# Kernel tuning notes

Hardware: AMD Instinct MI355X
Metric: run time of the kernel (lower is better)

Reference implementation:

```python
import jax, jax.numpy as jnp
import numpy as np

TOPK = (1, 5)


def setup_inputs() -> dict:
    key = jax.random.key(0)
    kZ, kY, kI = jax.random.split(key, 3)
    b, s, f = 9600, 2400, 4096
    Z = jax.random.normal(kZ, (b, f), dtype=jnp.float32)
    Y = jax.random.normal(kY, (s, f), dtype=jnp.float32)
    y_idxs = jax.random.randint(kI, (b,), 0, s, dtype=jnp.int64 if jax.config.jax_enable_x64 else jnp.int32)
    test_y_idxs = jnp.arange(s, dtype=y_idxs.dtype)
    return {"Z": Z, "y_idxs": y_idxs, "Y": Y, "test_y_idxs": test_y_idxs}


def reference(Z, y_idxs, Y, test_y_idxs):
    # L2-normalize rows, then cosine similarity as a single GEMM instead of the
    # original broadcasted (b, s, f) F.cosine_similarity intermediate.
    eps = 1e-8
    Zn = Z / jnp.maximum(jnp.linalg.norm(Z, axis=-1, keepdims=True), eps)
    Yn = Y / jnp.maximum(jnp.linalg.norm(Y, axis=-1, keepdims=True), eps)
    similarity = Zn @ Yn.T  # (b, s)

    # labels[i] = position of y_idxs[i] inside test_y_idxs (each appears exactly once)
    labels = jnp.argmax(y_idxs[None, :] == test_y_idxs[:, None], axis=0)  # (b,)

    accs = []
    for k in TOPK:
        _, topk_idx = jax.lax.top_k(similarity, k)  # (b, k)
        hit = jnp.any(topk_idx == labels[:, None], axis=1)
        accs.append(jnp.mean(hit.astype(jnp.float32)))
    return jnp.stack(accs)
```

## Files before the change

### kernel.cpp

```cpp
#include <hip/hip_runtime.h>

#define INT_MAX_C 0x7fffffff

typedef __attribute__((ext_vector_type(8))) short s16x8;
typedef __attribute__((ext_vector_type(4))) float f32x4;

__global__ void k_init_inv(int* inv, int s) {
  int j = blockIdx.x * 256 + threadIdx.x;
  if (j < s) inv[j] = INT_MAX_C;
}

__global__ void k_scatter(const int* __restrict__ tyi, int* __restrict__ inv, int s) {
  int j = blockIdx.x * 256 + threadIdx.x;
  if (j < s) {
    int v = tyi[j];
    if (v >= 0 && v < s) atomicMin(&inv[v], j);
  }
}

__global__ void k_labels(const int* __restrict__ yi, const int* __restrict__ inv,
                         int* __restrict__ labels, int b, int s) {
  int i = blockIdx.x * 256 + threadIdx.x;
  if (i < b) {
    int v = yi[i];
    int lab = 0;
    if (v >= 0 && v < s) { int p = inv[v]; if (p != INT_MAX_C) lab = p; }
    labels[i] = lab;
  }
}

__global__ __launch_bounds__(256) void k_ynorm(const float* __restrict__ Y,
                                               float* __restrict__ invY, int f) {
  int j = blockIdx.x;
  const float* row = Y + (size_t)j * f;
  float ss = 0.f;
  for (int k = threadIdx.x * 4; k < f; k += 256 * 4) {
    float4 v = *(const float4*)(row + k);
    ss += v.x * v.x + v.y * v.y + v.z * v.z + v.w * v.w;
  }
  int lane = threadIdx.x & 63, wid = threadIdx.x >> 6;
#pragma unroll
  for (int o = 32; o > 0; o >>= 1) ss += __shfl_down(ss, o, 64);
  __shared__ float sh[4];
  if (lane == 0) sh[wid] = ss;
  __syncthreads();
  if (threadIdx.x == 0) {
    float tot = sh[0] + sh[1] + sh[2] + sh[3];
    invY[j] = 1.f / fmaxf(sqrtf(tot), 1e-8f);
  }
}

__global__ __launch_bounds__(256) void k_zrow(
    const float* __restrict__ Z, const float* __restrict__ Y,
    const int* __restrict__ labels, const float* __restrict__ invY,
    float* __restrict__ invZ, float* __restrict__ simL, int f) {
  int i = blockIdx.x;
  int lab = labels[i];
  const float* zr = Z + (size_t)i * f;
  const float* yr = Y + (size_t)lab * f;
  float ss = 0.f, dt = 0.f;
  for (int k = threadIdx.x * 4; k < f; k += 256 * 4) {
    float4 z = *(const float4*)(zr + k);
    float4 y = *(const float4*)(yr + k);
    ss += z.x * z.x + z.y * z.y + z.z * z.z + z.w * z.w;
    dt += z.x * y.x + z.y * y.y + z.z * y.z + z.w * y.w;
  }
  int lane = threadIdx.x & 63, wid = threadIdx.x >> 6;
#pragma unroll
  for (int o = 32; o > 0; o >>= 1) {
    ss += __shfl_down(ss, o, 64);
    dt += __shfl_down(dt, o, 64);
  }
  __shared__ float shs[4], shd[4];
  if (lane == 0) { shs[wid] = ss; shd[wid] = dt; }
  __syncthreads();
  if (threadIdx.x == 0) {
    float S = shs[0] + shs[1] + shs[2] + shs[3];
    float D = shd[0] + shd[1] + shd[2] + shd[3];
    float iz = 1.f / fmaxf(sqrtf(S), 1e-8f);
    invZ[i] = iz;
    simL[i] = D * iz * invY[lab];
  }
}

__device__ __forceinline__ uint rne_hi_bits(uint u) {
  return (u + 0x7fffu + ((u >> 16) & 1u)) & 0xffff0000u;
}

__device__ __forceinline__ void split_pack8(float4 a, float4 b, uint4& hi, uint4& lo) {
  float v[8] = {a.x, a.y, a.z, a.w, b.x, b.y, b.z, b.w};
  uint h[8], l[8];
#pragma unroll
  for (int i = 0; i < 8; ++i) {
    uint u = __float_as_uint(v[i]);
    uint rh = rne_hi_bits(u);
    h[i] = rh;
    float d = v[i] - __uint_as_float(rh);
    uint ud = __float_as_uint(d);
    l[i] = (ud + 0x7fffu + ((ud >> 16) & 1u));
  }
  hi = make_uint4((h[0] >> 16) | h[1], (h[2] >> 16) | h[3],
                  (h[4] >> 16) | h[5], (h[6] >> 16) | h[7]);
  lo = make_uint4((l[0] >> 16) | (l[1] & 0xffff0000u),
                  (l[2] >> 16) | (l[3] & 0xffff0000u),
                  (l[4] >> 16) | (l[5] & 0xffff0000u),
                  (l[6] >> 16) | (l[7] & 0xffff0000u));
}

__global__ __launch_bounds__(256) void k_packZ(const float* __restrict__ Z,
                                               const float* __restrict__ Y,
                                               const int* __restrict__ labels,
                                               const float* __restrict__ invY,
                                               char* __restrict__ Zpan,
                                               float* __restrict__ invZ,
                                               float* __restrict__ simL,
                                               int f, int nkc) {
  int r = blockIdx.x * 4 + (threadIdx.x >> 6);
  int lane = threadIdx.x & 63;
  int rt = r >> 7, rl = r & 127;
  char* pan = Zpan + (size_t)rt * nkc * 16384;
  const float* row = Z + (size_t)r * f;
  int lab = labels[r];
  const float* yrow = Y + (size_t)lab * f;
  float ss = 0.f, dt = 0.f;
  int niter = f >> 9;
  for (int j = 0; j < niter; ++j) {
    int gq = lane + 64 * j;
    float4 v0 = *(const float4*)(row + gq * 8);
    float4 v1 = *(const float4*)(row + gq * 8 + 4);
    float4 y0 = *(const float4*)(yrow + gq * 8);
    float4 y1 = *(const float4*)(yrow + gq * 8 + 4);
    ss += v0.x * v0.x + v0.y * v0.y + v0.z * v0.z + v0.w * v0.w +
          v1.x * v1.x + v1.y * v1.y + v1.z * v1.z + v1.w * v1.w;
    dt += v0.x * y0.x + v0.y * y0.y + v0.z * y0.z + v0.w * y0.w +
          v1.x * y1.x + v1.y * y1.y + v1.z * y1.z + v1.w * y1.w;
    uint4 h, l;
    split_pack8(v0, v1, h, l);
    int kc = gq >> 2, kq = gq & 3;
    size_t off = (size_t)kc * 16384 + rl * 64 + ((kq ^ ((rl >> 1) & 3)) << 4);
    *(uint4*)(pan + off) = h;
    *(uint4*)(pan + off + 8192) = l;
  }
#pragma unroll
  for (int o = 32; o > 0; o >>= 1) {
    ss += __shfl_down(ss, o, 64);
    dt += __shfl_down(dt, o, 64);
  }
  if (lane == 0) {
    float iz = 1.f / fmaxf(sqrtf(ss), 1e-8f);
    invZ[r] = iz;
    simL[r] = dt * iz * invY[lab];
  }
}

__global__ __launch_bounds__(256) void k_packY(const float* __restrict__ Y,
                                               char* __restrict__ Ypan,
                                               float* __restrict__ invY,
                                               int s, int f, int nkc) {
  int r = blockIdx.x * 4 + (threadIdx.x >> 6);
  int lane = threadIdx.x & 63;
  int ct = r / 160, rl = r % 160;
  char* pan = Ypan + (size_t)ct * nkc * 20480;
  const float* row = Y + (size_t)r * f;
  const bool ok = r < s;
  float ss = 0.f;
  int niter = f >> 9;
  for (int j = 0; j < niter; ++j) {
    int gq = lane + 64 * j;
    float4 v0 = {}, v1 = {};
    if (ok) {
      v0 = *(const float4*)(row + gq * 8);
      v1 = *(const float4*)(row + gq * 8 + 4);
    }
    ss += v0.x * v0.x + v0.y * v0.y + v0.z * v0.z + v0.w * v0.w +
          v1.x * v1.x + v1.y * v1.y + v1.z * v1.z + v1.w * v1.w;
    uint4 h, l;
    split_pack8(v0, v1, h, l);
    int kc = gq >> 2, kq = gq & 3;
    size_t off = (size_t)kc * 20480 + rl * 64 + ((kq ^ ((rl >> 1) & 3)) << 4);
    *(uint4*)(pan + off) = h;
    *(uint4*)(pan + off + 10240) = l;
  }
  if (ok) {
#pragma unroll
    for (int o = 32; o > 0; o >>= 1) ss += __shfl_down(ss, o, 64);
    if (lane == 0) invY[r] = 1.f / fmaxf(sqrtf(ss), 1e-8f);
  }
}

__device__ __forceinline__ void dma16(const void* g, void* l) {
  __builtin_amdgcn_global_load_lds((const __attribute__((address_space(1))) unsigned int*)g,
                                   (__attribute__((address_space(3))) unsigned int*)l,
                                   16, 0, 0);
}

__global__ __launch_bounds__(256, 3) void k_gemm_rank_pan(
    const char* __restrict__ Zpan, const char* __restrict__ Ypan,
    const float* __restrict__ invZ, const float* __restrict__ invY,
    const float* __restrict__ simL, const int* __restrict__ labels,
    int* __restrict__ rank, int b, int s, int nkc) {
  __shared__ ushort SMu[18432];
  char* SMb = (char*)SMu;
  __shared__ float sL[128], sIz[128];
  __shared__ int sLab[128], sCnt[128];

  const int t = threadIdx.x;
  const int row0 = blockIdx.x * 128;
  const int col0 = blockIdx.y * 160;

  if (t < 128) {
    int gi = row0 + t;
    sL[t] = simL[gi]; sIz[t] = invZ[gi]; sLab[t] = labels[gi];
    sCnt[t] = 0;
  }

  const char* srcA = Zpan + (size_t)blockIdx.x * nkc * 16384 + t * 16;
  const char* srcB = Ypan + (size_t)blockIdx.y * nkc * 20480 + t * 16;

  const int lane = t & 63;
  const int wv = t >> 6;
  const int wr = wv >> 1, wc = wv & 1;
  const int fm = lane & 15, quad = lane >> 4;

  int aoff[4], boff[5];
#pragma unroll
  for (int i = 0; i < 4; ++i) {
    int r = wr * 64 + i * 16 + fm;
    aoff[i] = r * 64 + ((quad ^ ((r >> 1) & 3)) << 4);
  }
#pragma unroll
  for (int i = 0; i < 5; ++i) {
    int c = wc * 80 + i * 16 + fm;
    boff[i] = 16384 + c * 64 + ((quad ^ ((c >> 1) & 3)) << 4);
  }

  f32x4 acc[4][5] = {};

  for (int kt = 0; kt < nkc; ++kt) {
    __syncthreads();
#pragma unroll
    for (int j = 0; j < 4; ++j) dma16(srcA + j * 4096, SMb + j * 4096 + t * 16);
#pragma unroll
    for (int j = 0; j < 5; ++j) dma16(srcB + j * 4096, SMb + 16384 + j * 4096 + t * 16);
    srcA += 16384; srcB += 20480;
    __syncthreads();

    s16x8 ah[4], al[4];
#pragma unroll
    for (int i = 0; i < 4; ++i) {
      ah[i] = *(const s16x8*)(SMb + aoff[i]);
      al[i] = *(const s16x8*)(SMb + aoff[i] + 8192);
    }
#pragma unroll
    for (int cc = 0; cc < 5; ++cc) {
      s16x8 bh = *(const s16x8*)(SMb + boff[cc]);
      s16x8 bl = *(const s16x8*)(SMb + boff[cc] + 10240);
#pragma unroll
      for (int rr = 0; rr < 4; ++rr) {
        acc[rr][cc] = __builtin_amdgcn_mfma_f32_16x16x32_bf16(ah[rr], bh, acc[rr][cc], 0, 0, 0);
        acc[rr][cc] = __builtin_amdgcn_mfma_f32_16x16x32_bf16(ah[rr], bl, acc[rr][cc], 0, 0, 0);
        acc[rr][cc] = __builtin_amdgcn_mfma_f32_16x16x32_bf16(al[rr], bh, acc[rr][cc], 0, 0, 0);
      }
    }
  }

  float iYc[5];
#pragma unroll
  for (int c = 0; c < 5; ++c) {
    int gj = col0 + wc * 80 + c * 16 + fm;
    iYc[c] = (gj < s) ? invY[gj] : 0.f;
  }

#pragma unroll
  for (int rr = 0; rr < 4; ++rr) {
#pragma unroll
    for (int reg = 0; reg < 4; ++reg) {
      int li = wr * 64 + rr * 16 + quad * 4 + reg;
      float iz = sIz[li], sl = sL[li];
      int lab = sLab[li];
      int cnt = 0;
#pragma unroll
      for (int c = 0; c < 5; ++c) {
        int gj = col0 + wc * 80 + c * 16 + fm;
        if (gj < s && gj != lab) {
          float sim = acc[rr][c][reg] * iz * iYc[c];
          cnt += (sim > sl || (sim == sl && gj < lab)) ? 1 : 0;
        }
      }
      cnt += __shfl_down(cnt, 8, 16);
      cnt += __shfl_down(cnt, 4, 16);
      cnt += __shfl_down(cnt, 2, 16);
      cnt += __shfl_down(cnt, 1, 16);
      if (fm == 0 && cnt) atomicAdd(&sCnt[li], cnt);
    }
  }
  __syncthreads();
  if (t < 128) {
    int gi = row0 + t;
    if (sCnt[t]) atomicAdd(&rank[gi], sCnt[t]);
  }
}

#define TMF 128
#define TNF 128
#define BKF 32
#define SKF 40

__global__ __launch_bounds__(256) void k_gemm_rank_v2(
    const float* __restrict__ Z, const float* __restrict__ Y,
    const float* __restrict__ invZ, const float* __restrict__ invY,
    const float* __restrict__ simL, const int* __restrict__ labels,
    int* __restrict__ rank, int b, int s, int f) {
  __shared__ short Ah[TMF * SKF], Al[TMF * SKF], Bh[TNF * SKF], Bl[TNF * SKF];
  __shared__ float sL[TMF], sIz[TMF];
  __shared__ int sLab[TMF], sCnt[TMF];

  const int t = threadIdx.x;
  const int row0 = blockIdx.y * TMF;
  const int col0 = blockIdx.x * TNF;

  if (t < TMF) {
    int gi = row0 + t;
    if (gi < b) { sL[t] = simL[gi]; sIz[t] = invZ[gi]; sLab[t] = labels[gi]; }
    else        { sL[t] = 0.f;      sIz[t] = 0.f;      sLab[t] = -1; }
    sCnt[t] = 0;
  }

  const int srow  = t >> 1;
  const int skoff = (t & 1) << 4;
  const bool zok = (row0 + srow) < b;
  const bool yok = (col0 + srow) < s;
  const float* zp = Z + (size_t)(row0 + srow) * f + skoff;
  const float* yp = Y + (size_t)(col0 + srow) * f + skoff;

  const int lane = t & 63;
  const int wv = t >> 6;
  const int wr = wv >> 1, wc = wv & 1;
  const int fm = lane & 15, quad = lane >> 4;

  f32x4 acc[4][4] = {};

  for (int kt = 0; kt < f; kt += BKF) {
    float4 z0 = {}, z1 = {}, z2 = {}, z3 = {};
    float4 y0 = {}, y1 = {}, y2 = {}, y3 = {};
    if (zok) {
      z0 = *(const float4*)(zp + 0); z1 = *(const float4*)(zp + 4);
      z2 = *(const float4*)(zp + 8); z3 = *(const float4*)(zp + 12);
    }
    if (yok) {
      y0 = *(const float4*)(yp + 0); y1 = *(const float4*)(yp + 4);
      y2 = *(const float4*)(yp + 8); y3 = *(const float4*)(yp + 12);
    }
    zp += BKF; yp += BKF;

    __syncthreads();

    uint4 h, l;
    split_pack8(z0, z1, h, l);
    *(uint4*)(Ah + srow * SKF + skoff)     = h;
    *(uint4*)(Al + srow * SKF + skoff)     = l;
    split_pack8(z2, z3, h, l);
    *(uint4*)(Ah + srow * SKF + skoff + 8) = h;
    *(uint4*)(Al + srow * SKF + skoff + 8) = l;
    split_pack8(y0, y1, h, l);
    *(uint4*)(Bh + srow * SKF + skoff)     = h;
    *(uint4*)(Bl + srow * SKF + skoff)     = l;
    split_pack8(y2, y3, h, l);
    *(uint4*)(Bh + srow * SKF + skoff + 8) = h;
    *(uint4*)(Bl + srow * SKF + skoff + 8) = l;

    __syncthreads();

    s16x8 ah[4], al4[4], bh[4], bl4[4];
#pragma unroll
    for (int rr = 0; rr < 4; ++rr) {
      int ar = wr * 64 + rr * 16 + fm;
      ah[rr]  = *(const s16x8*)(Ah + ar * SKF + quad * 8);
      al4[rr] = *(const s16x8*)(Al + ar * SKF + quad * 8);
    }
#pragma unroll
    for (int cc = 0; cc < 4; ++cc) {
      int br = wc * 64 + cc * 16 + fm;
      bh[cc]  = *(const s16x8*)(Bh + br * SKF + quad * 8);
      bl4[cc] = *(const s16x8*)(Bl + br * SKF + quad * 8);
    }
#pragma unroll
    for (int rr = 0; rr < 4; ++rr)
#pragma unroll
      for (int cc = 0; cc < 4; ++cc) {
        acc[rr][cc] = __builtin_amdgcn_mfma_f32_16x16x32_bf16(ah[rr],  bh[cc],  acc[rr][cc], 0, 0, 0);
        acc[rr][cc] = __builtin_amdgcn_mfma_f32_16x16x32_bf16(ah[rr],  bl4[cc], acc[rr][cc], 0, 0, 0);
        acc[rr][cc] = __builtin_amdgcn_mfma_f32_16x16x32_bf16(al4[rr], bh[cc],  acc[rr][cc], 0, 0, 0);
      }
  }

  float iYc[4]; int gjc[4];
#pragma unroll
  for (int c = 0; c < 4; ++c) {
    int gj = col0 + wc * 64 + c * 16 + fm;
    gjc[c] = gj;
    iYc[c] = (gj < s) ? invY[gj] : 0.f;
  }

#pragma unroll
  for (int rr = 0; rr < 4; ++rr) {
#pragma unroll
    for (int reg = 0; reg < 4; ++reg) {
      int li = wr * 64 + rr * 16 + quad * 4 + reg;
      int gi = row0 + li;
      int cnt = 0;
      if (gi < b) {
        float iz = sIz[li], sl = sL[li];
        int lab = sLab[li];
#pragma unroll
        for (int c = 0; c < 4; ++c) {
          int gj = gjc[c];
          if (gj < s && gj != lab) {
            float sim = acc[rr][c][reg] * iz * iYc[c];
            cnt += (sim > sl || (sim == sl && gj < lab)) ? 1 : 0;
          }
        }
      }
      cnt += __shfl_down(cnt, 8, 16);
      cnt += __shfl_down(cnt, 4, 16);
      cnt += __shfl_down(cnt, 2, 16);
      cnt += __shfl_down(cnt, 1, 16);
      if (fm == 0 && cnt) atomicAdd(&sCnt[li], cnt);
    }
  }
  __syncthreads();
  if (t < TMF) {
    int gi = row0 + t;
    if (gi < b && sCnt[t]) atomicAdd(&rank[gi], sCnt[t]);
  }
}

__global__ __launch_bounds__(256) void k_final(const int* __restrict__ rank,
                                               float* __restrict__ out, int b) {
  int c1 = 0, c5 = 0;
  for (int i = threadIdx.x; i < b; i += 256) {
    int r = rank[i];
    c1 += (r < 1);
    c5 += (r < 5);
  }
  int lane = threadIdx.x & 63, wid = threadIdx.x >> 6;
#pragma unroll
  for (int o = 32; o > 0; o >>= 1) {
    c1 += __shfl_down(c1, o, 64);
    c5 += __shfl_down(c5, o, 64);
  }
  __shared__ int s1[4], s5[4];
  if (lane == 0) { s1[wid] = c1; s5[wid] = c5; }
  __syncthreads();
  if (threadIdx.x == 0) {
    int t1 = s1[0] + s1[1] + s1[2] + s1[3];
    int t5 = s5[0] + s5[1] + s5[2] + s5[3];
    out[0] = (float)t1 / (float)b;
    out[1] = (float)t5 / (float)b;
  }
}

extern "C" void kernel_launch(void* const* d_in, const int* in_sizes, int n_in,
                              void* d_out, int out_size, void* d_ws, size_t ws_size,
                              hipStream_t stream) {
  const float* Z  = (const float*)d_in[0];
  const int* yi   = (const int*)d_in[1];
  const float* Y  = (const float*)d_in[2];
  const int* tyi  = (const int*)d_in[3];
  const int b = in_sizes[1];
  const int s = in_sizes[3];
  const int f = in_sizes[0] / b;
  float* out = (float*)d_out;

  char* p = (char*)d_ws;
  size_t used = 0;
  auto alloc = [&](size_t bytes) {
    char* r = p;
    size_t a = (bytes + 255) & ~(size_t)255;
    p += a; used += a;
    return r;
  };
  int* inv     = (int*)alloc((size_t)s * 4);
  int* labels  = (int*)alloc((size_t)b * 4);
  int* rank    = (int*)alloc((size_t)b * 4);
  float* invY  = (float*)alloc((size_t)s * 4);
  float* invZ  = (float*)alloc((size_t)b * 4);
  float* simL  = (float*)alloc((size_t)b * 4);

  const int nkc = f >> 5;
  const int nrt = b / 128;
  const int nct = (s + 159) / 160;
  const int rows_pad = nct * 160;
  const size_t zpan_sz = (size_t)nrt * nkc * 16384;
  const size_t ypan_sz = (size_t)nct * nkc * 20480;
  const size_t need = used + zpan_sz + ypan_sz + 1024;
  const bool use_pan = (ws_size >= need) && (b % 128 == 0) && (f % 512 == 0);

  hipMemsetAsync(rank, 0, (size_t)b * 4, stream);
  k_init_inv<<<(s + 255) / 256, 256, 0, stream>>>(inv, s);
  k_scatter<<<(s + 255) / 256, 256, 0, stream>>>(tyi, inv, s);
  k_labels<<<(b + 255) / 256, 256, 0, stream>>>(yi, inv, labels, b, s);

  if (use_pan) {
    char* Zpan = (char*)alloc(zpan_sz);
    char* Ypan = (char*)alloc(ypan_sz);
    k_packY<<<rows_pad / 4, 256, 0, stream>>>(Y, Ypan, invY, s, f, nkc);
    k_packZ<<<b / 4, 256, 0, stream>>>(Z, Y, labels, invY, Zpan, invZ, simL, f, nkc);
    dim3 grid(nrt, nct);
    k_gemm_rank_pan<<<grid, 256, 0, stream>>>(Zpan, Ypan, invZ, invY, simL,
                                              labels, rank, b, s, nkc);
  } else {
    k_ynorm<<<s, 256, 0, stream>>>(Y, invY, f);
    k_zrow<<<b, 256, 0, stream>>>(Z, Y, labels, invY, invZ, simL, f);
    dim3 grid((s + TNF - 1) / TNF, (b + TMF - 1) / TMF);
    k_gemm_rank_v2<<<grid, 256, 0, stream>>>(Z, Y, invZ, invY, simL, labels,
                                             rank, b, s, f);
  }
  k_final<<<1, 256, 0, stream>>>(rank, out, b);
}
```

Before: 765.4 us.

## Switch GEMM to 32x32 MFMA tiles and fuse prep, pack and final kernels

The GEMM-rank kernel now uses 32x32x16 bf16 MFMA, with each wave owning 32 rows and all 160 columns of the block tile instead of a 2x2 wave grid of 16x16 tiles. This changes the LDS fragment reuse pattern and the epilogue reduction. The label-prep kernels are merged into one single-block launch, and the Z/Y packing kernels into one launch. The final accuracy reduction moves into the GEMM kernel through a last-block ticket, which removes several small launches. The trade-offs are more B-fragment LDS reads per wave and a serial tail in the last block.

Result: slower. 893.7 us (+16.8%).

```diff
diff --git a/kernel.cpp b/kernel.cpp
--- a/kernel.cpp
+++ b/kernel.cpp
@@ -4,24 +4,21 @@
 
 typedef __attribute__((ext_vector_type(8))) short s16x8;
 typedef __attribute__((ext_vector_type(4))) float f32x4;
-
-__global__ void k_init_inv(int* inv, int s) {
-  int j = blockIdx.x * 256 + threadIdx.x;
-  if (j < s) inv[j] = INT_MAX_C;
-}
-
-__global__ void k_scatter(const int* __restrict__ tyi, int* __restrict__ inv, int s) {
-  int j = blockIdx.x * 256 + threadIdx.x;
-  if (j < s) {
+typedef __attribute__((ext_vector_type(16))) float f32x16;
+
+__global__ __launch_bounds__(1024) void k_prep(const int* __restrict__ yi,
+                                               const int* __restrict__ tyi,
+                                               int* __restrict__ inv,
+                                               int* __restrict__ labels,
+                                               int b, int s) {
+  for (int j = threadIdx.x; j < s; j += 1024) inv[j] = INT_MAX_C;
+  __syncthreads();
+  for (int j = threadIdx.x; j < s; j += 1024) {
     int v = tyi[j];
     if (v >= 0 && v < s) atomicMin(&inv[v], j);
   }
-}
-
-__global__ void k_labels(const int* __restrict__ yi, const int* __restrict__ inv,
-                         int* __restrict__ labels, int b, int s) {
-  int i = blockIdx.x * 256 + threadIdx.x;
-  if (i < b) {
+  __syncthreads();
+  for (int i = threadIdx.x; i < b; i += 1024) {
     int v = yi[i];
     int lab = 0;
     if (v >= 0 && v < s) { int p = inv[v]; if (p != INT_MAX_C) lab = p; }
@@ -107,84 +104,79 @@
                   (l[6] >> 16) | (l[7] & 0xffff0000u));
 }
 
-__global__ __launch_bounds__(256) void k_packZ(const float* __restrict__ Z,
-                                               const float* __restrict__ Y,
-                                               const int* __restrict__ labels,
-                                               const float* __restrict__ invY,
-                                               char* __restrict__ Zpan,
-                                               float* __restrict__ invZ,
-                                               float* __restrict__ simL,
-                                               int f, int nkc) {
-  int r = blockIdx.x * 4 + (threadIdx.x >> 6);
+__global__ __launch_bounds__(256) void k_pack(const float* __restrict__ Z,
+                                              const float* __restrict__ Y,
+                                              const int* __restrict__ labels,
+                                              char* __restrict__ Zpan,
+                                              char* __restrict__ Ypan,
+                                              float* __restrict__ invZ,
+                                              float* __restrict__ dotL,
+                                              float* __restrict__ invY,
+                                              int s, int f, int nkc, int zblocks) {
   int lane = threadIdx.x & 63;
-  int rt = r >> 7, rl = r & 127;
-  char* pan = Zpan + (size_t)rt * nkc * 16384;
-  const float* row = Z + (size_t)r * f;
-  int lab = labels[r];
-  const float* yrow = Y + (size_t)lab * f;
-  float ss = 0.f, dt = 0.f;
   int niter = f >> 9;
-  for (int j = 0; j < niter; ++j) {
-    int gq = lane + 64 * j;
-    float4 v0 = *(const float4*)(row + gq * 8);
-    float4 v1 = *(const float4*)(row + gq * 8 + 4);
-    float4 y0 = *(const float4*)(yrow + gq * 8);
-    float4 y1 = *(const float4*)(yrow + gq * 8 + 4);
-    ss += v0.x * v0.x + v0.y * v0.y + v0.z * v0.z + v0.w * v0.w +
-          v1.x * v1.x + v1.y * v1.y + v1.z * v1.z + v1.w * v1.w;
-    dt += v0.x * y0.x + v0.y * y0.y + v0.z * y0.z + v0.w * y0.w +
-          v1.x * y1.x + v1.y * y1.y + v1.z * y1.z + v1.w * y1.w;
-    uint4 h, l;
-    split_pack8(v0, v1, h, l);
-    int kc = gq >> 2, kq = gq & 3;
-    size_t off = (size_t)kc * 16384 + rl * 64 + ((kq ^ ((rl >> 1) & 3)) << 4);
-    *(uint4*)(pan + off) = h;
-    *(uint4*)(pan + off + 8192) = l;
-  }
-#pragma unroll
-  for (int o = 32; o > 0; o >>= 1) {
-    ss += __shfl_down(ss, o, 64);
-    dt += __shfl_down(dt, o, 64);
-  }
-  if (lane == 0) {
-    float iz = 1.f / fmaxf(sqrtf(ss), 1e-8f);
-    invZ[r] = iz;
-    simL[r] = dt * iz * invY[lab];
-  }
-}
-
-__global__ __launch_bounds__(256) void k_packY(const float* __restrict__ Y,
-                                               char* __restrict__ Ypan,
-                                               float* __restrict__ invY,
-                                               int s, int f, int nkc) {
-  int r = blockIdx.x * 4 + (threadIdx.x >> 6);
-  int lane = threadIdx.x & 63;
-  int ct = r / 160, rl = r % 160;
-  char* pan = Ypan + (size_t)ct * nkc * 20480;
-  const float* row = Y + (size_t)r * f;
-  const bool ok = r < s;
-  float ss = 0.f;
-  int niter = f >> 9;
-  for (int j = 0; j < niter; ++j) {
-    int gq = lane + 64 * j;
-    float4 v0 = {}, v1 = {};
+  if ((int)blockIdx.x < zblocks) {
+    int r = blockIdx.x * 4 + (threadIdx.x >> 6);
+    int rt = r >> 7, rl = r & 127;
+    char* pan = Zpan + (size_t)rt * nkc * 16384;
+    const float* row = Z + (size_t)r * f;
+    int lab = labels[r];
+    const float* yrow = Y + (size_t)lab * f;
+    float ss = 0.f, dt = 0.f;
+    for (int j = 0; j < niter; ++j) {
+      int gq = lane + 64 * j;
+      float4 v0 = *(const float4*)(row + gq * 8);
+      float4 v1 = *(const float4*)(row + gq * 8 + 4);
+      float4 y0 = *(const float4*)(yrow + gq * 8);
+      float4 y1 = *(const float4*)(yrow + gq * 8 + 4);
+      ss += v0.x * v0.x + v0.y * v0.y + v0.z * v0.z + v0.w * v0.w +
+            v1.x * v1.x + v1.y * v1.y + v1.z * v1.z + v1.w * v1.w;
+      dt += v0.x * y0.x + v0.y * y0.y + v0.z * y0.z + v0.w * y0.w +
+            v1.x * y1.x + v1.y * y1.y + v1.z * y1.z + v1.w * y1.w;
+      uint4 h, l;
+      split_pack8(v0, v1, h, l);
+      int kc = gq >> 2, kq = gq & 3;
+      size_t off = (size_t)kc * 16384 + rl * 64 + ((kq ^ ((rl >> 1) & 3)) << 4);
+      *(uint4*)(pan + off) = h;
+      *(uint4*)(pan + off + 8192) = l;
+    }
+#pragma unroll
+    for (int o = 32; o > 0; o >>= 1) {
+      ss += __shfl_down(ss, o, 64);
+      dt += __shfl_down(dt, o, 64);
+    }
+    if (lane == 0) {
+      invZ[r] = 1.f / fmaxf(sqrtf(ss), 1e-8f);
+      dotL[r] = dt;
+    }
+  } else {
+    int r = (blockIdx.x - zblocks) * 4 + (threadIdx.x >> 6);
+    int ct = r / 160, rl = r % 160;
+    char* pan = Ypan + (size_t)ct * nkc * 20480;
+    const float* row = Y + (size_t)r * f;
+    const bool ok = r < s;
+    float ss = 0.f;
+    for (int j = 0; j < niter; ++j) {
+      int gq = lane + 64 * j;
+      float4 v0 = {}, v1 = {};
+      if (ok) {
+        v0 = *(const float4*)(row + gq * 8);
+        v1 = *(const float4*)(row + gq * 8 + 4);
+      }
+      ss += v0.x * v0.x + v0.y * v0.y + v0.z * v0.z + v0.w * v0.w +
+            v1.x * v1.x + v1.y * v1.y + v1.z * v1.z + v1.w * v1.w;
+      uint4 h, l;
+      split_pack8(v0, v1, h, l);
+      int kc = gq >> 2, kq = gq & 3;
+      size_t off = (size_t)kc * 20480 + rl * 64 + ((kq ^ ((rl >> 1) & 3)) << 4);
+      *(uint4*)(pan + off) = h;
+      *(uint4*)(pan + off + 10240) = l;
+    }
     if (ok) {
-      v0 = *(const float4*)(row + gq * 8);
-      v1 = *(const float4*)(row + gq * 8 + 4);
-    }
-    ss += v0.x * v0.x + v0.y * v0.y + v0.z * v0.z + v0.w * v0.w +
-          v1.x * v1.x + v1.y * v1.y + v1.z * v1.z + v1.w * v1.w;
-    uint4 h, l;
-    split_pack8(v0, v1, h, l);
-    int kc = gq >> 2, kq = gq & 3;
-    size_t off = (size_t)kc * 20480 + rl * 64 + ((kq ^ ((rl >> 1) & 3)) << 4);
-    *(uint4*)(pan + off) = h;
-    *(uint4*)(pan + off + 10240) = l;
-  }
-  if (ok) {
-#pragma unroll
-    for (int o = 32; o > 0; o >>= 1) ss += __shfl_down(ss, o, 64);
-    if (lane == 0) invY[r] = 1.f / fmaxf(sqrtf(ss), 1e-8f);
+#pragma unroll
+      for (int o = 32; o > 0; o >>= 1) ss += __shfl_down(ss, o, 64);
+      if (lane == 0) invY[r] = 1.f / fmaxf(sqrtf(ss), 1e-8f);
+    }
   }
 }
 
@@ -197,12 +189,15 @@
 __global__ __launch_bounds__(256, 3) void k_gemm_rank_pan(
     const char* __restrict__ Zpan, const char* __restrict__ Ypan,
     const float* __restrict__ invZ, const float* __restrict__ invY,
-    const float* __restrict__ simL, const int* __restrict__ labels,
-    int* __restrict__ rank, int b, int s, int nkc) {
+    const float* __restrict__ dotL, const int* __restrict__ labels,
+    int* __restrict__ rank, int* __restrict__ ticket, float* __restrict__ out,
+    int b, int s, int nkc, int nblocks) {
   __shared__ ushort SMu[18432];
   char* SMb = (char*)SMu;
   __shared__ float sL[128], sIz[128];
   __shared__ int sLab[128], sCnt[128];
+  __shared__ int sLast;
+  __shared__ int s1[4], s5[4];
 
   const int t = threadIdx.x;
   const int row0 = blockIdx.x * 128;
@@ -210,7 +205,11 @@
 
   if (t < 128) {
     int gi = row0 + t;
-    sL[t] = simL[gi]; sIz[t] = invZ[gi]; sLab[t] = labels[gi];
+    int lab = labels[gi];
+    float iz = invZ[gi];
+    sIz[t] = iz;
+    sLab[t] = lab;
+    sL[t] = dotL[gi] * iz * invY[lab];
     sCnt[t] = 0;
   }
 
@@ -219,22 +218,19 @@
 
   const int lane = t & 63;
   const int wv = t >> 6;
-  const int wr = wv >> 1, wc = wv & 1;
-  const int fm = lane & 15, quad = lane >> 4;
-
-  int aoff[4], boff[5];
-#pragma unroll
-  for (int i = 0; i < 4; ++i) {
-    int r = wr * 64 + i * 16 + fm;
-    aoff[i] = r * 64 + ((quad ^ ((r >> 1) & 3)) << 4);
-  }
-#pragma unroll
-  for (int i = 0; i < 5; ++i) {
-    int c = wc * 80 + i * 16 + fm;
-    boff[i] = 16384 + c * 64 + ((quad ^ ((c >> 1) & 3)) << 4);
-  }
-
-  f32x4 acc[4][5] = {};
+  const int ln = lane & 31;
+  const int h  = lane >> 5;
+  const int sw = (ln >> 1) & 3;
+
+  int aoff[2], boff[2];
+#pragma unroll
+  for (int kw = 0; kw < 2; ++kw) {
+    int ch = (((kw << 1) | h) ^ sw) << 4;
+    aoff[kw] = (wv * 32 + ln) * 64 + ch;
+    boff[kw] = 16384 + ln * 64 + ch;
+  }
+
+  f32x16 acc[5] = {};
 
   for (int kt = 0; kt < nkc; ++kt) {
     __syncthreads();
@@ -245,59 +241,84 @@
     srcA += 16384; srcB += 20480;
     __syncthreads();
 
-    s16x8 ah[4], al[4];
-#pragma unroll
-    for (int i = 0; i < 4; ++i) {
-      ah[i] = *(const s16x8*)(SMb + aoff[i]);
-      al[i] = *(const s16x8*)(SMb + aoff[i] + 8192);
-    }
+#pragma unroll
+    for (int kw = 0; kw < 2; ++kw) {
+      s16x8 ah = *(const s16x8*)(SMb + aoff[kw]);
+      s16x8 al = *(const s16x8*)(SMb + aoff[kw] + 8192);
+#pragma unroll
+      for (int cc = 0; cc < 5; ++cc) {
+        s16x8 bh = *(const s16x8*)(SMb + boff[kw] + cc * 2048);
+        s16x8 bl = *(const s16x8*)(SMb + boff[kw] + cc * 2048 + 10240);
+        acc[cc] = __builtin_amdgcn_mfma_f32_32x32x16_bf16(ah, bh, acc[cc], 0, 0, 0);
+        acc[cc] = __builtin_amdgcn_mfma_f32_32x32x16_bf16(ah, bl, acc[cc], 0, 0, 0);
+        acc[cc] = __builtin_amdgcn_mfma_f32_32x32x16_bf16(al, bh, acc[cc], 0, 0, 0);
+      }
+    }
+  }
+
+  float iY[5];
+#pragma unroll
+  for (int cc = 0; cc < 5; ++cc) {
+    int gj = col0 + cc * 32 + ln;
+    iY[cc] = (gj < s) ? invY[gj] : 0.f;
+  }
+
+#pragma unroll
+  for (int reg = 0; reg < 16; ++reg) {
+    int li = wv * 32 + (reg & 3) + 8 * (reg >> 2) + 4 * h;
+    float iz = sIz[li], sl = sL[li];
+    int lab = sLab[li];
+    int cnt = 0;
 #pragma unroll
     for (int cc = 0; cc < 5; ++cc) {
-      s16x8 bh = *(const s16x8*)(SMb + boff[cc]);
-      s16x8 bl = *(const s16x8*)(SMb + boff[cc] + 10240);
-#pragma unroll
-      for (int rr = 0; rr < 4; ++rr) {
-        acc[rr][cc] = __builtin_amdgcn_mfma_f32_16x16x32_bf16(ah[rr], bh, acc[rr][cc], 0, 0, 0);
-        acc[rr][cc] = __builtin_amdgcn_mfma_f32_16x16x32_bf16(ah[rr], bl, acc[rr][cc], 0, 0, 0);
-        acc[rr][cc] = __builtin_amdgcn_mfma_f32_16x16x32_bf16(al[rr], bh, acc[rr][cc], 0, 0, 0);
+      int gj = col0 + cc * 32 + ln;
+      if (gj < s && gj != lab) {
+        float sim = acc[cc][reg] * iz * iY[cc];
+        cnt += (sim > sl || (sim == sl && gj < lab)) ? 1 : 0;
       }
     }
-  }
-
-  float iYc[5];
-#pragma unroll
-  for (int c = 0; c < 5; ++c) {
-    int gj = col0 + wc * 80 + c * 16 + fm;
-    iYc[c] = (gj < s) ? invY[gj] : 0.f;
-  }
-
-#pragma unroll
-  for (int rr = 0; rr < 4; ++rr) {
-#pragma unroll
-    for (int reg = 0; reg < 4; ++reg) {
-      int li = wr * 64 + rr * 16 + quad * 4 + reg;
-      float iz = sIz[li], sl = sL[li];
-      int lab = sLab[li];
-      int cnt = 0;
-#pragma unroll
-      for (int c = 0; c < 5; ++c) {
-        int gj = col0 + wc * 80 + c * 16 + fm;
-        if (gj < s && gj != lab) {
-          float sim = acc[rr][c][reg] * iz * iYc[c];
-          cnt += (sim > sl || (sim == sl && gj < lab)) ? 1 : 0;
-        }
-      }
-      cnt += __shfl_down(cnt, 8, 16);
-      cnt += __shfl_down(cnt, 4, 16);
-      cnt += __shfl_down(cnt, 2, 16);
-      cnt += __shfl_down(cnt, 1, 16);
-      if (fm == 0 && cnt) atomicAdd(&sCnt[li], cnt);
-    }
+    cnt += __shfl_down(cnt, 16, 32);
+    cnt += __shfl_down(cnt, 8, 32);
+    cnt += __shfl_down(cnt, 4, 32);
+    cnt += __shfl_down(cnt, 2, 32);
+    cnt += __shfl_down(cnt, 1, 32);
+    if (ln == 0 && cnt) atomicAdd(&sCnt[li], cnt);
   }
   __syncthreads();
   if (t < 128) {
     int gi = row0 + t;
     if (sCnt[t]) atomicAdd(&rank[gi], sCnt[t]);
+  }
+  __syncthreads();
+
+  if (t == 0) {
+    __threadfence();
+    int v = atomicAdd(ticket, 1);
+    sLast = (v == nblocks - 1) ? 1 : 0;
+  }
+  __syncthreads();
+  if (sLast) {
+    __threadfence();
+    int c1 = 0, c5 = 0;
+    for (int i = t; i < b; i += 256) {
+      int r = atomicAdd(&rank[i], 0);
+      c1 += (r < 1);
+      c5 += (r < 5);
+    }
+    int wid = t >> 6;
+#pragma unroll
+    for (int o = 32; o > 0; o >>= 1) {
+      c1 += __shfl_down(c1, o, 64);
+      c5 += __shfl_down(c5, o, 64);
+    }
+    if (lane == 0) { s1[wid] = c1; s5[wid] = c5; }
+    __syncthreads();
+    if (t == 0) {
+      int t1 = s1[0] + s1[1] + s1[2] + s1[3];
+      int t5 = s5[0] + s5[1] + s5[2] + s5[3];
+      out[0] = (float)t1 / (float)b;
+      out[1] = (float)t5 / (float)b;
+    }
   }
 }
 
@@ -482,10 +503,11 @@
   };
   int* inv     = (int*)alloc((size_t)s * 4);
   int* labels  = (int*)alloc((size_t)b * 4);
-  int* rank    = (int*)alloc((size_t)b * 4);
+  int* rank    = (int*)alloc((size_t)b * 4 + 4);
+  int* ticket  = rank + b;
   float* invY  = (float*)alloc((size_t)s * 4);
   float* invZ  = (float*)alloc((size_t)b * 4);
-  float* simL  = (float*)alloc((size_t)b * 4);
+  float* dotL  = (float*)alloc((size_t)b * 4);
 
   const int nkc = f >> 5;
   const int nrt = b / 128;
@@ -496,25 +518,27 @@
   const size_t need = used + zpan_sz + ypan_sz + 1024;
   const bool use_pan = (ws_size >= need) && (b % 128 == 0) && (f % 512 == 0);
 
-  hipMemsetAsync(rank, 0, (size_t)b * 4, stream);
-  k_init_inv<<<(s + 255) / 256, 256, 0, stream>>>(inv, s);
-  k_scatter<<<(s + 255) / 256, 256, 0, stream>>>(tyi, inv, s);
-  k_labels<<<(b + 255) / 256, 256, 0, stream>>>(yi, inv, labels, b, s);
+  hipMemsetAsync(rank, 0, (size_t)b * 4 + 4, stream);
+  k_prep<<<1, 1024, 0, stream>>>(yi, tyi, inv, labels, b, s);
 
   if (use_pan) {
     char* Zpan = (char*)alloc(zpan_sz);
     char* Ypan = (char*)alloc(ypan_sz);
-    k_packY<<<rows_pad / 4, 256, 0, stream>>>(Y, Ypan, invY, s, f, nkc);
-    k_packZ<<<b / 4, 256, 0, stream>>>(Z, Y, labels, invY, Zpan, invZ, simL, f, nkc);
+    const int zblocks = b / 4;
+    const int yblocks = rows_pad / 4;
+    k_pack<<<zblocks + yblocks, 256, 0, stream>>>(Z, Y, labels, Zpan, Ypan,
+                                                  invZ, dotL, invY, s, f, nkc,
+                                                  zblocks);
     dim3 grid(nrt, nct);
-    k_gemm_rank_pan<<<grid, 256, 0, stream>>>(Zpan, Ypan, invZ, invY, simL,
-                                              labels, rank, b, s, nkc);
+    k_gemm_rank_pan<<<grid, 256, 0, stream>>>(Zpan, Ypan, invZ, invY, dotL,
+                                              labels, rank, ticket, out,
+                                              b, s, nkc, nrt * nct);
   } else {
     k_ynorm<<<s, 256, 0, stream>>>(Y, invY, f);
-    k_zrow<<<b, 256, 0, stream>>>(Z, Y, labels, invY, invZ, simL, f);
+    k_zrow<<<b, 256, 0, stream>>>(Z, Y, labels, invY, invZ, dotL, f);
     dim3 grid((s + TNF - 1) / TNF, (b + TMF - 1) / TMF);
-    k_gemm_rank_v2<<<grid, 256, 0, stream>>>(Z, Y, invZ, invY, simL, labels,
+    k_gemm_rank_v2<<<grid, 256, 0, stream>>>(Z, Y, invZ, invY, dotL, labels,
                                              rank, b, s, f);
-  }
-  k_final<<<1, 256, 0, stream>>>(rank, out, b);
-}
+    k_final<<<1, 256, 0, stream>>>(rank, out, b);
+  }
+}
```
